# Kernel tuning notes

Hardware: AMD Instinct MI355X
Metric: run time of the kernel (lower is better)

Reference implementation:

```python
import jax, jax.numpy as jnp
import numpy as np

K = 9  # kernel_size (knn neighbors, loop=True -> self included)

def setup_inputs() -> dict:
    key = jax.random.key(0)
    k1, k2, k3 = jax.random.split(key, 3)
    B, C, H, W = 8, 64, 32, 32
    OUT = 64
    x = jax.random.normal(k1, (B, C, H, W), dtype=jnp.float32)
    # SAGEConv params: lin_l (neighbor aggregate, with bias), lin_r (root, no bias)
    s = 1.0 / np.sqrt(C)
    W_l = jax.random.uniform(k2, (OUT, C), minval=-s, maxval=s, dtype=jnp.float32)
    b_l = jnp.zeros((OUT,), dtype=jnp.float32)
    W_r = jax.random.uniform(k3, (OUT, C), minval=-s, maxval=s, dtype=jnp.float32)
    return {"x": x, "W_l": W_l, "b_l": b_l, "W_r": W_r}

def _knn_mean(x_f, batches):
    # squared-euclidean pairwise distances [N, N], masked across batches
    sq = jnp.sum(x_f * x_f, axis=-1)
    dist = sq[:, None] + sq[None, :] - 2.0 * (x_f @ x_f.T)
    cross = batches[:, None] != batches[None, :]
    dist = jnp.where(cross, jnp.inf, dist)
    neg, idx = jax.lax.top_k(-dist, K)          # k nearest (self included, dist 0)
    valid = (neg != -jnp.inf).astype(x_f.dtype)  # handle degenerate last-batch node
    nbr = x_f[idx] * valid[..., None]            # [N, K, C]
    return nbr.sum(axis=1) / valid.sum(axis=1, keepdims=True)

def reference(x, W_l, b_l, W_r):
    B, C, H, Wd = x.shape
    N = B * H * Wd
    x_f = x.transpose(0, 2, 3, 1).reshape(N, C)  # flat_nodes: [B*H*W, C]
    # torch.linspace(0, B, steps=N).to(int64): truncation of i*B/(N-1)
    batches = jnp.linspace(0.0, float(B), N).astype(jnp.int32)
    mean_nbr = _knn_mean(x_f, batches)
    # SAGEConv: lin_l(mean_j x_j) + lin_r(x_i)
    return mean_nbr @ W_l.T + b_l + x_f @ W_r.T
```

## Files before the change

### kernel.cpp

```cpp
#include <hip/hip_runtime.h>
#include <cstdint>
#include <cstddef>


__global__ __launch_bounds__(256, 4) void k_all(const float* __restrict__ x,
                                                const float* __restrict__ Wl,
                                                const float* __restrict__ bl,
                                                const float* __restrict__ Wr,
                                                float* __restrict__ out) {
  __shared__ float SH[9728];
  float* Xs = SH;
  float* Asf = SH + 8192;
  float* sqX = SH + 8704;
  float4* Xs4 = (float4*)Xs;
  float4* sqX4 = (float4*)sqX;

  int bi = (int)blockIdx.x, t = threadIdx.x;
  int lane = t & 63, w = t >> 6;
  int n0 = bi << 3;
  int s = (n0 >= 7168) ? 7168 : (n0 & ~1023);
  const float* xb = x + (((size_t)(s >> 10)) << 16);
  const float* xrow = x + (((size_t)(n0 >> 10)) << 16) + (n0 & 1023);

  if (t < 128) {
    int ch = t >> 1, hf = t & 1;
    *(float4*)&Asf[(ch << 3) + (hf << 2)] =
        *(const float4*)&xrow[((size_t)ch << 10) + (hf << 2)];
  }

  float acc[2][16];
#pragma unroll
  for (int r = 0; r < 2; ++r)
#pragma unroll
    for (int c = 0; c < 16; ++c) acc[r][c] = 0.f;
  float4 p4 = {0.f, 0.f, 0.f, 0.f};

#pragma unroll 1
  for (int ks = 0; ks < 8; ++ks) {
    if (ks) __syncthreads();
    int k0 = ks << 3;
#pragma unroll
    for (int i = 0; i < 8; ++i) {
      int lin = t + (i << 8);
      int kc = lin >> 8, j4 = lin & 255;
      Xs4[(kc << 8) + j4] =
          *(const float4*)&xb[((size_t)(k0 + kc) << 10) + (j4 << 2)];
    }
    __syncthreads();
#pragma unroll
    for (int kc = 0; kc < 8; ++kc) {
      float4 v = Xs4[(kc << 8) + t];
      p4.x = fmaf(v.x, v.x, p4.x);
      p4.y = fmaf(v.y, v.y, p4.y);
      p4.z = fmaf(v.z, v.z, p4.z);
      p4.w = fmaf(v.w, v.w, p4.w);
    }
#pragma unroll
    for (int kc = 0; kc < 8; ++kc) {
      float2 a = *(const float2*)&Asf[((k0 + kc) << 3) + (w << 1)];
      float4 b0 = Xs4[(kc << 8) + lane];
      float4 b1 = Xs4[(kc << 8) + 64 + lane];
      float4 b2 = Xs4[(kc << 8) + 128 + lane];
      float4 b3 = Xs4[(kc << 8) + 192 + lane];
      float bv[16] = {b0.x, b0.y, b0.z, b0.w, b1.x, b1.y, b1.z, b1.w,
                      b2.x, b2.y, b2.z, b2.w, b3.x, b3.y, b3.z, b3.w};
#pragma unroll
      for (int c = 0; c < 16; ++c) {
        acc[0][c] = fmaf(a.x, bv[c], acc[0][c]);
        acc[1][c] = fmaf(a.y, bv[c], acc[1][c]);
      }
    }
  }
  sqX4[t] = p4;
  __syncthreads();

  float4 sq4[4];
#pragma unroll
  for (int q = 0; q < 4; ++q) sq4[q] = sqX4[(q << 6) + lane];

  float msum[2], xr[2];
  int cnt[2];
#pragma unroll 2
  for (int rr = 0; rr < 2; ++rr) {
    int n = n0 + (w << 1) + rr;
    float xself = x[(((size_t)(n >> 10)) << 16) + ((size_t)lane << 10) + (n & 1023)];
    xr[rr] = xself;
    if (n == 8191) {
      msum[rr] = xself;
      cnt[rr] = 1;
    } else {
      cnt[rr] = 9;
      float si = sqX[n - s];
      bool mlast = (n >= 7168);
      unsigned long long cand[16];
#pragma unroll
      for (int q = 0; q < 4; ++q) {
        float sj[4] = {sq4[q].x, sq4[q].y, sq4[q].z, sq4[q].w};
#pragma unroll
        for (int e = 0; e < 4; ++e) {
          float d = (si + sj[e]) - 2.f * acc[rr][(q << 2) + e];
          unsigned u = __float_as_uint(d);
          u = (u & 0x80000000u) ? ~u : (u | 0x80000000u);
          unsigned jj = (unsigned)((q << 8) + (lane << 2) + e);
          cand[(q << 2) + e] = ((unsigned long long)u << 32) | jj;
        }
      }
      if (mlast && lane == 63) cand[15] = ~0ull;
      unsigned long long m1 = cand[0], m2 = cand[1];
      if (m2 < m1) { unsigned long long tt = m1; m1 = m2; m2 = tt; }
#pragma unroll
      for (int q = 2; q < 16; ++q) {
        unsigned long long c = cand[q];
        unsigned long long lo = (c < m1) ? c : m1;
        unsigned long long hi = (c < m1) ? m1 : c;
        m2 = (hi < m2) ? hi : m2;
        m1 = lo;
      }
      unsigned long long lm = m1;
      unsigned rmask = 0;
      bool stale = false;
      unsigned jloc[9];
#pragma unroll
      for (int kk = 0; kk < 9; ++kk) {
        unsigned long long g = lm;
#pragma unroll
        for (int off = 32; off; off >>= 1) {
          unsigned ghi = __shfl_xor((unsigned)(g >> 32), off, 64);
          unsigned glo = __shfl_xor((unsigned)g, off, 64);
          unsigned long long o = ((unsigned long long)ghi << 32) | glo;
          g = (o < g) ? o : g;
        }
        jloc[kk] = (unsigned)g & 1023u;
        if (lm == g) {
          unsigned slot = (((unsigned)g >> 6) & 12u) | ((unsigned)g & 3u);
          rmask |= 1u << slot;
          if (!stale) { lm = m2; stale = true; }
          else {
            unsigned long long best = ~0ull;
#pragma unroll
            for (int q = 0; q < 16; ++q) {
              bool alive = ((rmask >> q) & 1u) == 0u;
              unsigned long long c = cand[q];
              best = (alive && c < best) ? c : best;
            }
            lm = best;
          }
        }
      }
      const float* gx = xb + ((size_t)lane << 10);
      float g0 = gx[jloc[0]], g1 = gx[jloc[1]], g2 = gx[jloc[2]];
      float g3 = gx[jloc[3]], g4 = gx[jloc[4]], g5 = gx[jloc[5]];
      float g6 = gx[jloc[6]], g7 = gx[jloc[7]], g8 = gx[jloc[8]];
      msum[rr] = (((g0 + g1) + (g2 + g3)) + ((g4 + g5) + (g6 + g7))) + g8;
    }
  }
  __syncthreads();

#pragma unroll
  for (int i = 0; i < 16; ++i) {
    int lin = t + (i << 8);
    int o = lin >> 6, c = lin & 63;
    SH[o * 65 + c] = Wl[lin];
    SH[4160 + o * 65 + c] = Wr[lin];
  }
  __syncthreads();

  float bias = bl[lane];
  float ms[2];
#pragma unroll
  for (int rr = 0; rr < 2; ++rr)
    ms[rr] = (cnt[rr] == 9) ? msum[rr] * (1.f / 9.f) : msum[rr];
  float accL[2] = {0.f, 0.f};
  float accR[2] = {0.f, 0.f};
#pragma unroll
  for (int c = 0; c < 64; ++c) {
    float wlc = SH[lane * 65 + c];
    float wrc = SH[4160 + lane * 65 + c];
#pragma unroll
    for (int rr = 0; rr < 2; ++rr) {
      float mc = __int_as_float(__builtin_amdgcn_readlane(__float_as_int(ms[rr]), c));
      float xc = __int_as_float(__builtin_amdgcn_readlane(__float_as_int(xr[rr]), c));
      accL[rr] = fmaf(mc, wlc, accL[rr]);
      accR[rr] = fmaf(xc, wrc, accR[rr]);
    }
  }
#pragma unroll
  for (int rr = 0; rr < 2; ++rr)
    __builtin_nontemporal_store(accL[rr] + accR[rr] + bias,
                                &out[((size_t)(n0 + (w << 1) + rr) << 6) + lane]);
}

extern "C" void kernel_launch(void* const* d_in, const int* in_sizes, int n_in,
                              void* d_out, int out_size, void* d_ws, size_t ws_size,
                              hipStream_t stream) {
  const float* x  = (const float*)d_in[0];
  const float* Wl = (const float*)d_in[1];
  const float* bl = (const float*)d_in[2];
  const float* Wr = (const float*)d_in[3];
  float* out = (float*)d_out;
  (void)d_ws; (void)ws_size;

  k_all<<<dim3(1024), 256, 0, stream>>>(x, Wl, bl, Wr, out);
}
```

Before: 108.5 us.

## Process 16 query rows per block, stream candidates from global directly

Each block now handles 16 query nodes (4 per wave) instead of 8, so the 1024-candidate tile is read half as many times across the grid. The shared-memory staging loop and its barriers are removed, and each lane loads its candidate columns straight from global memory into registers. The candidate squared norms are now computed in registers, and the query's own norm is pulled out with a select chain plus readlane. The accumulator array doubles to 4x16 and launch bounds drop to 2 blocks per CU. This trades occupancy and register pressure for less redundant loading and fewer barriers.

```diff
diff --git a/kernel.cpp b/kernel.cpp
--- a/kernel.cpp
+++ b/kernel.cpp
@@ -3,102 +3,85 @@
 #include <cstddef>
 
 
-__global__ __launch_bounds__(256, 4) void k_all(const float* __restrict__ x,
+__global__ __launch_bounds__(256, 2) void k_all(const float* __restrict__ x,
                                                 const float* __restrict__ Wl,
                                                 const float* __restrict__ bl,
                                                 const float* __restrict__ Wr,
                                                 float* __restrict__ out) {
-  __shared__ float SH[9728];
-  float* Xs = SH;
-  float* Asf = SH + 8192;
-  float* sqX = SH + 8704;
-  float4* Xs4 = (float4*)Xs;
-  float4* sqX4 = (float4*)sqX;
+  __shared__ float SH[8320];
+  float4* Asf4 = (float4*)SH;
 
   int bi = (int)blockIdx.x, t = threadIdx.x;
   int lane = t & 63, w = t >> 6;
-  int n0 = bi << 3;
+  int n0 = bi << 4;
   int s = (n0 >= 7168) ? 7168 : (n0 & ~1023);
-  const float* xb = x + (((size_t)(s >> 10)) << 16);
-  const float* xrow = x + (((size_t)(n0 >> 10)) << 16) + (n0 & 1023);
+  const float* xb = x + ((size_t)(s >> 10) << 16);
+  const float* xrow = x + ((size_t)(n0 >> 10) << 16) + (n0 & 1023);
 
-  if (t < 128) {
-    int ch = t >> 1, hf = t & 1;
-    *(float4*)&Asf[(ch << 3) + (hf << 2)] =
-        *(const float4*)&xrow[((size_t)ch << 10) + (hf << 2)];
+  {
+    int ch = t >> 2, g = t & 3;
+    Asf4[t] = *(const float4*)&xrow[((size_t)ch << 10) + (g << 2)];
+  }
+  __syncthreads();
+
+  float4 av = Asf4[(lane << 2) + w];
+
+  float acc[4][16];
+  float sqa[16];
+#pragma unroll
+  for (int r = 0; r < 4; ++r)
+#pragma unroll
+    for (int j = 0; j < 16; ++j) acc[r][j] = 0.f;
+#pragma unroll
+  for (int j = 0; j < 16; ++j) sqa[j] = 0.f;
+
+  const float* xl = xb + (lane << 2);
+#pragma unroll 4
+  for (int ch = 0; ch < 64; ++ch) {
+    float4 a4 = Asf4[(ch << 2) + w];
+    const float* xc = xl + ((size_t)ch << 10);
+    float4 b0 = *(const float4*)&xc[0];
+    float4 b1 = *(const float4*)&xc[256];
+    float4 b2 = *(const float4*)&xc[512];
+    float4 b3 = *(const float4*)&xc[768];
+    float bv[16] = {b0.x, b0.y, b0.z, b0.w, b1.x, b1.y, b1.z, b1.w,
+                    b2.x, b2.y, b2.z, b2.w, b3.x, b3.y, b3.z, b3.w};
+    float ar[4] = {a4.x, a4.y, a4.z, a4.w};
+#pragma unroll
+    for (int j = 0; j < 16; ++j) {
+      sqa[j] = fmaf(bv[j], bv[j], sqa[j]);
+      acc[0][j] = fmaf(ar[0], bv[j], acc[0][j]);
+      acc[1][j] = fmaf(ar[1], bv[j], acc[1][j]);
+      acc[2][j] = fmaf(ar[2], bv[j], acc[2][j]);
+      acc[3][j] = fmaf(ar[3], bv[j], acc[3][j]);
+    }
   }
 
-  float acc[2][16];
-#pragma unroll
-  for (int r = 0; r < 2; ++r)
-#pragma unroll
-    for (int c = 0; c < 16; ++c) acc[r][c] = 0.f;
-  float4 p4 = {0.f, 0.f, 0.f, 0.f};
-
-#pragma unroll 1
-  for (int ks = 0; ks < 8; ++ks) {
-    if (ks) __syncthreads();
-    int k0 = ks << 3;
-#pragma unroll
-    for (int i = 0; i < 8; ++i) {
-      int lin = t + (i << 8);
-      int kc = lin >> 8, j4 = lin & 255;
-      Xs4[(kc << 8) + j4] =
-          *(const float4*)&xb[((size_t)(k0 + kc) << 10) + (j4 << 2)];
-    }
-    __syncthreads();
-#pragma unroll
-    for (int kc = 0; kc < 8; ++kc) {
-      float4 v = Xs4[(kc << 8) + t];
-      p4.x = fmaf(v.x, v.x, p4.x);
-      p4.y = fmaf(v.y, v.y, p4.y);
-      p4.z = fmaf(v.z, v.z, p4.z);
-      p4.w = fmaf(v.w, v.w, p4.w);
-    }
-#pragma unroll
-    for (int kc = 0; kc < 8; ++kc) {
-      float2 a = *(const float2*)&Asf[((k0 + kc) << 3) + (w << 1)];
-      float4 b0 = Xs4[(kc << 8) + lane];
-      float4 b1 = Xs4[(kc << 8) + 64 + lane];
-      float4 b2 = Xs4[(kc << 8) + 128 + lane];
-      float4 b3 = Xs4[(kc << 8) + 192 + lane];
-      float bv[16] = {b0.x, b0.y, b0.z, b0.w, b1.x, b1.y, b1.z, b1.w,
-                      b2.x, b2.y, b2.z, b2.w, b3.x, b3.y, b3.z, b3.w};
-#pragma unroll
-      for (int c = 0; c < 16; ++c) {
-        acc[0][c] = fmaf(a.x, bv[c], acc[0][c]);
-        acc[1][c] = fmaf(a.y, bv[c], acc[1][c]);
-      }
-    }
-  }
-  sqX4[t] = p4;
-  __syncthreads();
-
-  float4 sq4[4];
-#pragma unroll
-  for (int q = 0; q < 4; ++q) sq4[q] = sqX4[(q << 6) + lane];
-
-  float msum[2], xr[2];
-  int cnt[2];
-#pragma unroll 2
-  for (int rr = 0; rr < 2; ++rr) {
-    int n = n0 + (w << 1) + rr;
-    float xself = x[(((size_t)(n >> 10)) << 16) + ((size_t)lane << 10) + (n & 1023)];
-    xr[rr] = xself;
+  float msum[4];
+  int cnt[4];
+#pragma unroll 4
+  for (int rr = 0; rr < 4; ++rr) {
+    int n = n0 + (w << 2) + rr;
+    float xself = (rr == 0) ? av.x : (rr == 1) ? av.y : (rr == 2) ? av.z : av.w;
     if (n == 8191) {
       msum[rr] = xself;
       cnt[rr] = 1;
     } else {
       cnt[rr] = 9;
-      float si = sqX[n - s];
+      int ln = n - s;
+      int slot_o = ((ln >> 8) << 2) | (ln & 3);
+      float sv = sqa[0];
+#pragma unroll
+      for (int j = 1; j < 16; ++j) sv = (slot_o == j) ? sqa[j] : sv;
+      float si = __int_as_float(
+          __builtin_amdgcn_readlane(__float_as_int(sv), (ln & 255) >> 2));
       bool mlast = (n >= 7168);
       unsigned long long cand[16];
 #pragma unroll
       for (int q = 0; q < 4; ++q) {
-        float sj[4] = {sq4[q].x, sq4[q].y, sq4[q].z, sq4[q].w};
 #pragma unroll
         for (int e = 0; e < 4; ++e) {
-          float d = (si + sj[e]) - 2.f * acc[rr][(q << 2) + e];
+          float d = (si + sqa[(q << 2) + e]) - 2.f * acc[rr][(q << 2) + e];
           unsigned u = __float_as_uint(d);
           u = (u & 0x80000000u) ? ~u : (u | 0x80000000u);
           unsigned jj = (unsigned)((q << 8) + (lane << 2) + e);
@@ -166,18 +149,19 @@
   __syncthreads();
 
   float bias = bl[lane];
-  float ms[2];
+  float ms[4];
 #pragma unroll
-  for (int rr = 0; rr < 2; ++rr)
+  for (int rr = 0; rr < 4; ++rr)
     ms[rr] = (cnt[rr] == 9) ? msum[rr] * (1.f / 9.f) : msum[rr];
-  float accL[2] = {0.f, 0.f};
-  float accR[2] = {0.f, 0.f};
+  float xr[4] = {av.x, av.y, av.z, av.w};
+  float accL[4] = {0.f, 0.f, 0.f, 0.f};
+  float accR[4] = {0.f, 0.f, 0.f, 0.f};
 #pragma unroll
   for (int c = 0; c < 64; ++c) {
     float wlc = SH[lane * 65 + c];
     float wrc = SH[4160 + lane * 65 + c];
 #pragma unroll
-    for (int rr = 0; rr < 2; ++rr) {
+    for (int rr = 0; rr < 4; ++rr) {
       float mc = __int_as_float(__builtin_amdgcn_readlane(__float_as_int(ms[rr]), c));
       float xc = __int_as_float(__builtin_amdgcn_readlane(__float_as_int(xr[rr]), c));
       accL[rr] = fmaf(mc, wlc, accL[rr]);
@@ -185,9 +169,9 @@
     }
   }
 #pragma unroll
-  for (int rr = 0; rr < 2; ++rr)
+  for (int rr = 0; rr < 4; ++rr)
     __builtin_nontemporal_store(accL[rr] + accR[rr] + bias,
-                                &out[((size_t)(n0 + (w << 1) + rr) << 6) + lane]);
+                                &out[((size_t)(n0 + (w << 2) + rr) << 6) + lane]);
 }
 
 extern "C" void kernel_launch(void* const* d_in, const int* in_sizes, int n_in,
@@ -200,5 +184,5 @@
   float* out = (float*)d_out;
   (void)d_ws; (void)ws_size;
 
-  k_all<<<dim3(1024), 256, 0, stream>>>(x, Wl, bl, Wr, out);
+  k_all<<<dim3(512), 256, 0, stream>>>(x, Wl, bl, Wr, out);
 }
```

Result: no change. 107.0 us (-1.4%).
